# Performance work log

Hardware: AMD Instinct MI355X
Metric: run time of the kernel (lower is better)

## Reference

```python
import jax, jax.numpy as jnp
import numpy as np

D_MODEL = 1024
N_HEADS = 16
D_K = D_MODEL // N_HEADS
ROPE_THETA = 10000.0


def setup_inputs() -> dict:
    key = jax.random.key(0)
    ks = jax.random.split(key, 5)
    B, S = 2, 2048
    scale = 1.0 / np.sqrt(D_MODEL)
    return {
        "x": jax.random.normal(ks[0], (B, S, D_MODEL), dtype=jnp.float32),
        "token_positions": jnp.arange(S, dtype=jnp.int32),
        "Wq": jax.random.normal(ks[1], (D_MODEL, D_MODEL), dtype=jnp.float32) * scale,
        "Wk": jax.random.normal(ks[2], (D_MODEL, D_MODEL), dtype=jnp.float32) * scale,
        "Wv": jax.random.normal(ks[3], (D_MODEL, D_MODEL), dtype=jnp.float32) * scale,
        "Wo": jax.random.normal(ks[4], (D_MODEL, D_MODEL), dtype=jnp.float32) * scale,
    }


def apply_rope(x, positions):
    # x: [b, h, s, d_k]; interleaved-pair rotary embedding, theta=10000
    half = D_K // 2
    inv_freq = ROPE_THETA ** (-jnp.arange(0, half, dtype=x.dtype) * 2.0 / D_K)  # [half]
    angles = positions.astype(x.dtype)[:, None] * inv_freq[None, :]             # [s, half]
    cos, sin = jnp.cos(angles), jnp.sin(angles)                                 # [s, half]
    x1 = x[..., 0::2]
    x2 = x[..., 1::2]
    r1 = x1 * cos - x2 * sin
    r2 = x1 * sin + x2 * cos
    # re-interleave
    return jnp.stack([r1, r2], axis=-1).reshape(x.shape)


def reference(x, token_positions, Wq, Wk, Wv, Wo):
    B, S, _ = x.shape
    # Linear(d_model, d_model) with no bias: y = x @ W.T
    Q = jnp.einsum("bsd,ed->bse", x, Wq).reshape(B, S, N_HEADS, D_K).transpose(0, 2, 1, 3)
    K = jnp.einsum("bsd,ed->bse", x, Wk).reshape(B, S, N_HEADS, D_K).transpose(0, 2, 1, 3)
    V = jnp.einsum("bsd,ed->bse", x, Wv).reshape(B, S, N_HEADS, D_K).transpose(0, 2, 1, 3)
    Q = apply_rope(Q, token_positions)
    K = apply_rope(K, token_positions)
    scores = jnp.einsum("bhqd,bhkd->bhqk", Q, K) / jnp.sqrt(jnp.asarray(D_K, x.dtype))
    causal = jnp.tril(jnp.ones((S, S), dtype=bool))
    scores = jnp.where(causal[None, None, :, :], scores, jnp.asarray(-jnp.inf, x.dtype))
    attn = jax.nn.softmax(scores, axis=-1)
    out = jnp.einsum("bhqk,bhkd->bhqd", attn, V)            # [b, h, s, d_k]
    out = out.transpose(0, 2, 1, 3).reshape(B, S, D_MODEL)   # [b, s, d_model]
    return jnp.einsum("bsd,ed->bse", out, Wo)
```

## Files before the change

kernel.cpp:

```cpp
#include <hip/hip_runtime.h>
#include <math.h>

#define SEQ 2048
#define NH  16
#define DKH 64
#define DM  1024
#define MR  4096

using bf16x8 = __attribute__((ext_vector_type(8))) short;
using f32x4  = __attribute__((ext_vector_type(4))) float;

__device__ __forceinline__ ushort f2b(float f) {
  unsigned u = __float_as_uint(f);
  return (ushort)((u + 0x7fffu + ((u >> 16) & 1u)) >> 16);
}

__device__ __forceinline__ void gll16(const void* g, void* l) {
  __builtin_amdgcn_global_load_lds(
      (const __attribute__((address_space(1))) void*)g,
      (__attribute__((address_space(3))) void*)l, 16, 0, 0);
}

__global__ __launch_bounds__(256) void cvt_all(
    const float* __restrict__ x,  const float* __restrict__ wq,
    const float* __restrict__ wk, const float* __restrict__ wv,
    const float* __restrict__ wo,
    ushort* __restrict__ xb,  ushort* __restrict__ wqb, ushort* __restrict__ wkb,
    ushort* __restrict__ wvb, ushort* __restrict__ wob)
{
  size_t e = ((size_t)blockIdx.x * 256 + threadIdx.x) * 4;
  const float* s; ushort* d; size_t off;
  if      (e < 4194304) { s = x;  d = xb;  off = e; }
  else if (e < 5242880) { s = wq; d = wqb; off = e - 4194304; }
  else if (e < 6291456) { s = wk; d = wkb; off = e - 5242880; }
  else if (e < 7340032) { s = wv; d = wvb; off = e - 6291456; }
  else                  { s = wo; d = wob; off = e - 7340032; }
  float4 f = *(const float4*)(s + off);
  ushort4 o4 = { f2b(f.x), f2b(f.y), f2b(f.z), f2b(f.w) };
  *(ushort4*)(d + off) = o4;
}

__global__ __launch_bounds__(512) void gemm_qkv(
    const ushort* __restrict__ X,
    const ushort* __restrict__ Wq, const ushort* __restrict__ Wk, const ushort* __restrict__ Wv,
    ushort* __restrict__ Q, ushort* __restrict__ K, ushort* __restrict__ Vt,
    const int* __restrict__ pos)
{
  __shared__ __align__(16) char As[2][16384];
  __shared__ __align__(16) char Bs[2][16384];

  const int id  = blockIdx.x;
  const int xcd = id & 7;
  const int i   = id >> 3;
  const int mt  = xcd * 4 + (i & 3);
  const int nt  = i >> 2;
  const int m0  = mt * 128;
  const int nG  = nt * 128;
  const int z   = nG >> 10;
  const int n0  = nG & 1023;
  const ushort* W = (z == 0) ? Wq : (z == 1) ? Wk : Wv;

  const int tid  = threadIdx.x;
  const int lane = tid & 63;
  const int w    = tid >> 6;
  const int wm   = (w >> 2) * 64;
  const int wn   = (w & 3) * 32;
  const int li   = lane & 15;
  const int g    = lane >> 4;

  f32x4 acc[4][2] = {};

  auto stage = [&](int t, int buf) {
    const int k0 = t * 64;
    #pragma unroll
    for (int it = 0; it < 2; ++it) {
      const int L  = w * 2048 + it * 1024 + lane * 16;
      const int r  = L >> 7;
      const int sc = ((L >> 4) & 7) ^ (r & 7);
      gll16(X + (size_t)(m0 + r) * DM + k0 + sc * 8, &As[buf][w * 2048 + it * 1024]);
      gll16(W + (size_t)(n0 + r) * DM + k0 + sc * 8, &Bs[buf][w * 2048 + it * 1024]);
    }
  };

  auto compute = [&](int buf) {
    #pragma unroll
    for (int ks = 0; ks < 2; ++ks) {
      bf16x8 af[4], bfr[2];
      #pragma unroll
      for (int mf = 0; mf < 4; ++mf) {
        const int row = wm + mf * 16 + li;
        af[mf] = *(const bf16x8*)(&As[buf][row * 128 + (((ks * 4 + g) ^ (row & 7)) << 4)]);
      }
      #pragma unroll
      for (int nf = 0; nf < 2; ++nf) {
        const int row = wn + nf * 16 + li;
        bfr[nf] = *(const bf16x8*)(&Bs[buf][row * 128 + (((ks * 4 + g) ^ (row & 7)) << 4)]);
      }
      #pragma unroll
      for (int mf = 0; mf < 4; ++mf)
        #pragma unroll
        for (int nf = 0; nf < 2; ++nf)
          acc[mf][nf] = __builtin_amdgcn_mfma_f32_16x16x32_bf16(af[mf], bfr[nf], acc[mf][nf], 0, 0, 0);
    }
  };

  stage(0, 0);
  for (int t = 0; t < 16; ++t) {
    if (t < 15) {
      stage(t + 1, (t + 1) & 1);
      __builtin_amdgcn_sched_barrier(0);
      asm volatile("s_waitcnt vmcnt(4)" ::: "memory");
    } else {
      asm volatile("s_waitcnt vmcnt(0)" ::: "memory");
    }
    __builtin_amdgcn_s_barrier();
    __builtin_amdgcn_sched_barrier(0);
    compute(t & 1);
    __builtin_amdgcn_sched_barrier(0);
    __builtin_amdgcn_s_barrier();
  }

  #pragma unroll
  for (int nf = 0; nf < 2; ++nf) {
    const int n = n0 + wn + nf * 16 + li;
    const int h = n >> 6;
    const int d = n & 63;
    if (z == 2) {
      #pragma unroll
      for (int mf = 0; mf < 4; ++mf) {
        const int m  = m0 + wm + mf * 16 + g * 4;
        const int b  = m >> 11;
        const int s2 = m & (SEQ - 1);
        ushort4 pk = { f2b(acc[mf][nf][0]), f2b(acc[mf][nf][1]),
                       f2b(acc[mf][nf][2]), f2b(acc[mf][nf][3]) };
        *(ushort4*)(Vt + (((size_t)b * NH + h) * DKH + d) * SEQ + s2) = pk;
      }
    } else {
      ushort* DST = (z == 0) ? Q : K;
      const float freq = __expf(-(float)(d >> 1) * 0.2878231366242557f);
      #pragma unroll
      for (int mf = 0; mf < 4; ++mf) {
        #pragma unroll
        for (int r = 0; r < 4; ++r) {
          const int m  = m0 + wm + mf * 16 + g * 4 + r;
          const int b  = m >> 11;
          const int s2 = m & (SEQ - 1);
          const float ang = (float)pos[s2] * freq;
          float sn, cs;
          __sincosf(ang, &sn, &cs);
          const float v1 = acc[mf][nf][r];
          const float v2 = __shfl_xor(v1, 1);
          float ov = (d & 1) ? (v2 * sn + v1 * cs)
                             : (v1 * cs - v2 * sn);
          if (z == 0) ov *= 0.125f;
          DST[(((size_t)b * NH + h) * SEQ + s2) * DKH + d] = f2b(ov);
        }
      }
    }
  }
}

__global__ __launch_bounds__(512) void gemm_wo(
    const ushort* __restrict__ A, const ushort* __restrict__ W,
    float* __restrict__ out)
{
  __shared__ __align__(16) char As[2][16384];
  __shared__ __align__(16) char Bs[2][16384];

  const int id  = blockIdx.x;
  const int xcd = id & 7;
  const int i   = id >> 3;
  const int mt  = xcd * 4 + (i & 3);
  const int nt  = i >> 2;
  const int m0  = mt * 128;
  const int n0  = nt * 128;

  const int tid  = threadIdx.x;
  const int lane = tid & 63;
  const int w    = tid >> 6;
  const int wm   = (w >> 2) * 64;
  const int wn   = (w & 3) * 32;
  const int li   = lane & 15;
  const int g    = lane >> 4;

  f32x4 acc[4][2] = {};

  auto stage = [&](int t, int buf) {
    const int k0 = t * 64;
    #pragma unroll
    for (int it = 0; it < 2; ++it) {
      const int L  = w * 2048 + it * 1024 + lane * 16;
      const int r  = L >> 7;
      const int sc = ((L >> 4) & 7) ^ (r & 7);
      gll16(A + (size_t)(m0 + r) * DM + k0 + sc * 8, &As[buf][w * 2048 + it * 1024]);
      gll16(W + (size_t)(n0 + r) * DM + k0 + sc * 8, &Bs[buf][w * 2048 + it * 1024]);
    }
  };

  auto compute = [&](int buf) {
    #pragma unroll
    for (int ks = 0; ks < 2; ++ks) {
      bf16x8 af[4], bfr[2];
      #pragma unroll
      for (int mf = 0; mf < 4; ++mf) {
        const int row = wm + mf * 16 + li;
        af[mf] = *(const bf16x8*)(&As[buf][row * 128 + (((ks * 4 + g) ^ (row & 7)) << 4)]);
      }
      #pragma unroll
      for (int nf = 0; nf < 2; ++nf) {
        const int row = wn + nf * 16 + li;
        bfr[nf] = *(const bf16x8*)(&Bs[buf][row * 128 + (((ks * 4 + g) ^ (row & 7)) << 4)]);
      }
      #pragma unroll
      for (int mf = 0; mf < 4; ++mf)
        #pragma unroll
        for (int nf = 0; nf < 2; ++nf)
          acc[mf][nf] = __builtin_amdgcn_mfma_f32_16x16x32_bf16(af[mf], bfr[nf], acc[mf][nf], 0, 0, 0);
    }
  };

  stage(0, 0);
  for (int t = 0; t < 16; ++t) {
    if (t < 15) {
      stage(t + 1, (t + 1) & 1);
      __builtin_amdgcn_sched_barrier(0);
      asm volatile("s_waitcnt vmcnt(4)" ::: "memory");
    } else {
      asm volatile("s_waitcnt vmcnt(0)" ::: "memory");
    }
    __builtin_amdgcn_s_barrier();
    __builtin_amdgcn_sched_barrier(0);
    compute(t & 1);
    __builtin_amdgcn_sched_barrier(0);
    __builtin_amdgcn_s_barrier();
  }

  #pragma unroll
  for (int nf = 0; nf < 2; ++nf)
    #pragma unroll
    for (int mf = 0; mf < 4; ++mf)
      #pragma unroll
      for (int r = 0; r < 4; ++r)
        out[(size_t)(m0 + wm + mf * 16 + g * 4 + r) * DM + n0 + wn + nf * 16 + li] = acc[mf][nf][r];
}

__global__ __launch_bounds__(256) void attn(
    const ushort* __restrict__ Q, const ushort* __restrict__ K,
    const ushort* __restrict__ Vt, ushort* __restrict__ AO)
{
  __shared__ __align__(16) char KsB[2][8192];
  __shared__ __align__(16) char VsB[2][8192];
  __shared__ __align__(16) char Ps[8192];

  const int tid  = threadIdx.x;
  const int lane = tid & 63;
  const int w    = tid >> 6;
  const int li   = lane & 15;
  const int g    = lane >> 4;

  const int bx  = blockIdx.x;
  const int xcd = bx & 7;
  const int idx = bx >> 3;
  const int bh  = (idx & 3) * 8 + xcd;
  const int qb  = 31 - (idx >> 2);
  const int q0b = qb * 64;
  const int n   = qb + 1;
  const int q0w = q0b + w * 16;

  const ushort* Qb = Q  + (size_t)bh * SEQ * DKH;
  const ushort* Kb = K  + (size_t)bh * SEQ * DKH;
  const ushort* Vb = Vt + (size_t)bh * DKH * SEQ;
  char* Pw = Ps + w * 2048;

  const bf16x8 qf0 = *(const bf16x8*)(Qb + (size_t)(q0w + li) * DKH + g * 8);
  const bf16x8 qf1 = *(const bf16x8*)(Qb + (size_t)(q0w + li) * DKH + 32 + g * 8);

  f32x4 o[4] = {};
  float m_ = -INFINITY, l_ = 0.f;

  auto stage = [&](int kt, int buf) {
    const int k0 = kt * 64;
    #pragma unroll
    for (int it = 0; it < 2; ++it) {
      const int L  = w * 2048 + it * 1024 + lane * 16;
      const int r  = L >> 7;
      const int sc = ((L >> 4) & 7) ^ (r & 7);
      gll16(Kb + (size_t)(k0 + r) * DKH + sc * 8, &KsB[buf][w * 2048 + it * 1024]);
      gll16(Vb + (size_t)r * SEQ + k0 + sc * 8,   &VsB[buf][w * 2048 + it * 1024]);
    }
  };

  auto computeT = [&](int t) {
    const int k0 = t * 64;
    const char* Kc = KsB[t & 1];
    const char* Vc = VsB[t & 1];

    f32x4 st[4] = {};
    #pragma unroll
    for (int nf = 0; nf < 4; ++nf) {
      const int row = nf * 16 + li;
      bf16x8 kfa = *(const bf16x8*)(Kc + row * 128 + (((0 + g) ^ (row & 7)) << 4));
      bf16x8 kfb = *(const bf16x8*)(Kc + row * 128 + (((4 + g) ^ (row & 7)) << 4));
      st[nf] = __builtin_amdgcn_mfma_f32_16x16x32_bf16(kfa, qf0, st[nf], 0, 0, 0);
      st[nf] = __builtin_amdgcn_mfma_f32_16x16x32_bf16(kfb, qf1, st[nf], 0, 0, 0);
    }

    #pragma unroll
    for (int nf = 0; nf < 4; ++nf)
      #pragma unroll
      for (int r = 0; r < 4; ++r)
        if (k0 + nf * 16 + g * 4 + r > q0w + li) st[nf][r] = -1e30f;

    float mx = fmaxf(fmaxf(fmaxf(st[0][0], st[0][1]), fmaxf(st[0][2], st[0][3])),
                     fmaxf(fmaxf(st[1][0], st[1][1]), fmaxf(st[1][2], st[1][3])));
    mx = fmaxf(mx, fmaxf(fmaxf(fmaxf(st[2][0], st[2][1]), fmaxf(st[2][2], st[2][3])),
                         fmaxf(fmaxf(st[3][0], st[3][1]), fmaxf(st[3][2], st[3][3]))));
    mx = fmaxf(mx, __shfl_xor(mx, 16));
    mx = fmaxf(mx, __shfl_xor(mx, 32));
    const float newm = fmaxf(m_, mx);
    const float al = __expf(m_ - newm);
    m_ = newm;

    float p[4][4];
    float rs = 0.f;
    #pragma unroll
    for (int nf = 0; nf < 4; ++nf)
      #pragma unroll
      for (int r = 0; r < 4; ++r) {
        p[nf][r] = __expf(st[nf][r] - newm);
        rs += p[nf][r];
      }
    rs += __shfl_xor(rs, 16);
    rs += __shfl_xor(rs, 32);
    l_ = l_ * al + rs;

    float alr[4];
    #pragma unroll
    for (int r = 0; r < 4; ++r) alr[r] = __shfl(al, g * 4 + r);
    #pragma unroll
    for (int nf = 0; nf < 4; ++nf)
      #pragma unroll
      for (int r = 0; r < 4; ++r) o[nf][r] *= alr[r];

    #pragma unroll
    for (int nf = 0; nf < 4; ++nf) {
      ushort4 pk = { f2b(p[nf][0]), f2b(p[nf][1]), f2b(p[nf][2]), f2b(p[nf][3]) };
      const int cw = nf * 2 + (g >> 1);
      *(ushort4*)(Pw + li * 128 + ((cw ^ (li & 7)) << 4) + ((g & 1) << 3)) = pk;
    }
    bf16x8 pf0 = *(const bf16x8*)(Pw + li * 128 + (((0 + g) ^ (li & 7)) << 4));
    bf16x8 pf1 = *(const bf16x8*)(Pw + li * 128 + (((4 + g) ^ (li & 7)) << 4));

    #pragma unroll
    for (int nf = 0; nf < 4; ++nf) {
      const int row = nf * 16 + li;
      bf16x8 vfa = *(const bf16x8*)(Vc + row * 128 + (((0 + g) ^ (row & 7)) << 4));
      bf16x8 vfb = *(const bf16x8*)(Vc + row * 128 + (((4 + g) ^ (row & 7)) << 4));
      o[nf] = __builtin_amdgcn_mfma_f32_16x16x32_bf16(pf0, vfa, o[nf], 0, 0, 0);
      o[nf] = __builtin_amdgcn_mfma_f32_16x16x32_bf16(pf1, vfb, o[nf], 0, 0, 0);
    }
  };

  stage(0, 0);
  for (int t = 0; t < n; ++t) {
    if (t + 1 < n) {
      stage(t + 1, (t + 1) & 1);
      __builtin_amdgcn_sched_barrier(0);
      asm volatile("s_waitcnt vmcnt(4)" ::: "memory");
    } else {
      asm volatile("s_waitcnt vmcnt(0)" ::: "memory");
    }
    __builtin_amdgcn_s_barrier();
    __builtin_amdgcn_sched_barrier(0);
    if (t * 64 <= q0w + 15) computeT(t);
    __builtin_amdgcn_sched_barrier(0);
    __builtin_amdgcn_s_barrier();
  }

  const float inv = 1.0f / l_;
  float ir[4];
  #pragma unroll
  for (int r = 0; r < 4; ++r) ir[r] = __shfl(inv, g * 4 + r);

  const int b = bh >> 4, h = bh & 15;
  #pragma unroll
  for (int nf = 0; nf < 4; ++nf)
    #pragma unroll
    for (int r = 0; r < 4; ++r) {
      const int q = q0w + g * 4 + r;
      AO[((size_t)b * SEQ + q) * DM + h * DKH + nf * 16 + li] = f2b(o[nf][r] * ir[r]);
    }
}

extern "C" void kernel_launch(void* const* d_in, const int* in_sizes, int n_in,
                              void* d_out, int out_size, void* d_ws, size_t ws_size,
                              hipStream_t stream)
{
  const float* x   = (const float*)d_in[0];
  const int*   pos = (const int*)  d_in[1];
  const float* Wq  = (const float*)d_in[2];
  const float* Wk  = (const float*)d_in[3];
  const float* Wv  = (const float*)d_in[4];
  const float* Wo  = (const float*)d_in[5];
  float* out = (float*)d_out;

  ushort* ws  = (ushort*)d_ws;
  ushort* xb  = ws;
  ushort* wqb = xb  + 4194304;
  ushort* wkb = wqb + 1048576;
  ushort* wvb = wkb + 1048576;
  ushort* wob = wvb + 1048576;
  ushort* Qb  = wob + 1048576;
  ushort* Kb  = Qb  + 4194304;
  ushort* Vtb = Kb  + 4194304;
  ushort* AOb = Vtb + 4194304;

  cvt_all<<<8192, 256, 0, stream>>>(x, Wq, Wk, Wv, Wo, xb, wqb, wkb, wvb, wob);
  gemm_qkv<<<768, 512, 0, stream>>>(xb, wqb, wkb, wvb, Qb, Kb, Vtb, pos);
  attn<<<1024, 256, 0, stream>>>(Qb, Kb, Vtb, AOb);
  gemm_wo<<<256, 512, 0, stream>>>(AOb, wob, out);
}
```

Before: 116.0 us.

## Streamline attention softmax with exp2, lazy rescaling, diagonal-only masking and balanced scheduling

```diff
diff --git a/kernel.cpp b/kernel.cpp
--- a/kernel.cpp
+++ b/kernel.cpp
@@ -13,6 +13,15 @@
 __device__ __forceinline__ ushort f2b(float f) {
   unsigned u = __float_as_uint(f);
   return (ushort)((u + 0x7fffu + ((u >> 16) & 1u)) >> 16);
+}
+
+__device__ __forceinline__ float exp2_fast(float x) {
+  float r; asm("v_exp_f32 %0, %1" : "=v"(r) : "v"(x)); return r;
+}
+
+__device__ __forceinline__ unsigned cvt_pk(float lo, float hi) {
+  unsigned r; asm("v_cvt_pk_bf16_f32 %0, %1, %2" : "=v"(r) : "v"(lo), "v"(hi));
+  return r;
 }
 
 __device__ __forceinline__ void gll16(const void* g, void* l) {
@@ -152,7 +161,7 @@
           const float v2 = __shfl_xor(v1, 1);
           float ov = (d & 1) ? (v2 * sn + v1 * cs)
                              : (v1 * cs - v2 * sn);
-          if (z == 0) ov *= 0.125f;
+          if (z == 0) ov *= 0.1803368801111204f;
           DST[(((size_t)b * NH + h) * SEQ + s2) * DKH + d] = f2b(ov);
         }
       }
@@ -261,8 +270,10 @@
   const int bx  = blockIdx.x;
   const int xcd = bx & 7;
   const int idx = bx >> 3;
-  const int bh  = (idx & 3) * 8 + xcd;
-  const int qb  = 31 - (idx >> 2);
+  const int j   = idx >> 2;
+  const int s   = idx & 3;
+  const int qb  = (s & 1) ? (31 - j) : j;
+  const int bh  = s * 8 + xcd;
   const int q0b = qb * 64;
   const int n   = qb + 1;
   const int q0w = q0b + w * 16;
@@ -290,12 +301,13 @@
     }
   };
 
-  auto computeT = [&](int t) {
+  auto computeT = [&](int t, bool diag) {
     const int k0 = t * 64;
     const char* Kc = KsB[t & 1];
     const char* Vc = VsB[t & 1];
 
     f32x4 st[4] = {};
+    __builtin_amdgcn_s_setprio(1);
     #pragma unroll
     for (int nf = 0; nf < 4; ++nf) {
       const int row = nf * 16 + li;
@@ -304,12 +316,15 @@
       st[nf] = __builtin_amdgcn_mfma_f32_16x16x32_bf16(kfa, qf0, st[nf], 0, 0, 0);
       st[nf] = __builtin_amdgcn_mfma_f32_16x16x32_bf16(kfb, qf1, st[nf], 0, 0, 0);
     }
-
-    #pragma unroll
-    for (int nf = 0; nf < 4; ++nf)
-      #pragma unroll
-      for (int r = 0; r < 4; ++r)
-        if (k0 + nf * 16 + g * 4 + r > q0w + li) st[nf][r] = -1e30f;
+    __builtin_amdgcn_s_setprio(0);
+
+    if (diag) {
+      #pragma unroll
+      for (int nf = 0; nf < 4; ++nf)
+        #pragma unroll
+        for (int r = 0; r < 4; ++r)
+          if (k0 + nf * 16 + g * 4 + r > q0w + li) st[nf][r] = -1e30f;
+    }
 
     float mx = fmaxf(fmaxf(fmaxf(st[0][0], st[0][1]), fmaxf(st[0][2], st[0][3])),
                      fmaxf(fmaxf(st[1][0], st[1][1]), fmaxf(st[1][2], st[1][3])));
@@ -317,9 +332,14 @@
                          fmaxf(fmaxf(st[3][0], st[3][1]), fmaxf(st[3][2], st[3][3]))));
     mx = fmaxf(mx, __shfl_xor(mx, 16));
     mx = fmaxf(mx, __shfl_xor(mx, 32));
-    const float newm = fmaxf(m_, mx);
-    const float al = __expf(m_ - newm);
-    m_ = newm;
+
+    const bool rescale = !__all(mx - m_ <= 8.0f);
+    float al = 1.0f;
+    if (rescale) {
+      const float newm = fmaxf(m_, mx);
+      al = exp2_fast(m_ - newm);
+      m_ = newm;
+    }
 
     float p[4][4];
     float rs = 0.f;
@@ -327,30 +347,35 @@
     for (int nf = 0; nf < 4; ++nf)
       #pragma unroll
       for (int r = 0; r < 4; ++r) {
-        p[nf][r] = __expf(st[nf][r] - newm);
+        p[nf][r] = exp2_fast(st[nf][r] - m_);
         rs += p[nf][r];
       }
     rs += __shfl_xor(rs, 16);
     rs += __shfl_xor(rs, 32);
-    l_ = l_ * al + rs;
-
-    float alr[4];
-    #pragma unroll
-    for (int r = 0; r < 4; ++r) alr[r] = __shfl(al, g * 4 + r);
-    #pragma unroll
-    for (int nf = 0; nf < 4; ++nf)
-      #pragma unroll
-      for (int r = 0; r < 4; ++r) o[nf][r] *= alr[r];
+
+    if (rescale) {
+      l_ = l_ * al + rs;
+      float alr[4];
+      #pragma unroll
+      for (int r = 0; r < 4; ++r) alr[r] = __shfl(al, g * 4 + r);
+      #pragma unroll
+      for (int nf = 0; nf < 4; ++nf)
+        #pragma unroll
+        for (int r = 0; r < 4; ++r) o[nf][r] *= alr[r];
+    } else {
+      l_ += rs;
+    }
 
     #pragma unroll
     for (int nf = 0; nf < 4; ++nf) {
-      ushort4 pk = { f2b(p[nf][0]), f2b(p[nf][1]), f2b(p[nf][2]), f2b(p[nf][3]) };
+      uint2 pv = { cvt_pk(p[nf][0], p[nf][1]), cvt_pk(p[nf][2], p[nf][3]) };
       const int cw = nf * 2 + (g >> 1);
-      *(ushort4*)(Pw + li * 128 + ((cw ^ (li & 7)) << 4) + ((g & 1) << 3)) = pk;
+      *(uint2*)(Pw + li * 128 + ((cw ^ (li & 7)) << 4) + ((g & 1) << 3)) = pv;
     }
     bf16x8 pf0 = *(const bf16x8*)(Pw + li * 128 + (((0 + g) ^ (li & 7)) << 4));
     bf16x8 pf1 = *(const bf16x8*)(Pw + li * 128 + (((4 + g) ^ (li & 7)) << 4));
 
+    __builtin_amdgcn_s_setprio(1);
     #pragma unroll
     for (int nf = 0; nf < 4; ++nf) {
       const int row = nf * 16 + li;
@@ -359,6 +384,7 @@
       o[nf] = __builtin_amdgcn_mfma_f32_16x16x32_bf16(pf0, vfa, o[nf], 0, 0, 0);
       o[nf] = __builtin_amdgcn_mfma_f32_16x16x32_bf16(pf1, vfb, o[nf], 0, 0, 0);
     }
+    __builtin_amdgcn_s_setprio(0);
   };
 
   stage(0, 0);
@@ -372,7 +398,7 @@
     }
     __builtin_amdgcn_s_barrier();
     __builtin_amdgcn_sched_barrier(0);
-    if (t * 64 <= q0w + 15) computeT(t);
+    computeT(t, t == n - 1);
     __builtin_amdgcn_sched_barrier(0);
     __builtin_amdgcn_s_barrier();
   }
```

Measured after the change: 113.6 us. -2.1%, faster.
